# Performance work log

Measured on AMD Instinct MI355X. Metric: run time of the kernel, lower is better.

Reference implementation:

```python
import jax, jax.numpy as jnp
import numpy as np

N = 100000      # nodes
E = 1600000     # directed edges (before self loops)
F_IN = 3        # node_feature_dim
H = 32          # hidden_dim
BN_EPS = 1e-5


def _linear_params(k, fan_in, fan_out):
    lim = 1.0 / np.sqrt(fan_in)
    kw, kb = jax.random.split(k)
    W = jax.random.uniform(kw, (fan_in, fan_out), jnp.float32, -lim, lim)
    b = jax.random.uniform(kb, (fan_out,), jnp.float32, -lim, lim)
    return W, b


def setup_inputs() -> dict:
    key = jax.random.key(0)
    ks = jax.random.split(key, 12)
    x = jax.random.normal(ks[0], (N, F_IN), jnp.float32)
    edge_index = jax.random.randint(ks[1], (2, E), 0, N, dtype=jnp.int64)
    node_type = jax.random.randint(ks[2], (N,), 0, 3, dtype=jnp.int64)
    W1, b1 = _linear_params(ks[3], F_IN, H)
    W2, b2 = _linear_params(ks[4], H, H)
    W3, b3 = _linear_params(ks[5], H, H)
    g1 = jnp.ones((H,), jnp.float32); be1 = jnp.zeros((H,), jnp.float32)
    g2 = jnp.ones((H,), jnp.float32); be2 = jnp.zeros((H,), jnp.float32)
    Wc1, bc1 = _linear_params(ks[6], H, H // 2)
    Wc2, bc2 = _linear_params(ks[7], H // 2, 1)
    Wd1, bd1 = _linear_params(ks[8], H, H // 2)
    Wd2, bd2 = _linear_params(ks[9], H // 2, 1)
    return dict(x=x, edge_index=edge_index, node_type=node_type,
                W1=W1, b1=b1, W2=W2, b2=b2, W3=W3, b3=b3,
                g1=g1, be1=be1, g2=g2, be2=be2,
                Wc1=Wc1, bc1=bc1, Wc2=Wc2, bc2=bc2,
                Wd1=Wd1, bd1=bd1, Wd2=Wd2, bd2=bd2)


def reference(x, edge_index, node_type, W1, b1, W2, b2, W3, b3,
              g1, be1, g2, be2, Wc1, bc1, Wc2, bc2, Wd1, bd1, Wd2, bd2):
    n = x.shape[0]
    # GCNConv (PyG default): add self loops, symmetric deg^-1/2 normalization
    loop = jnp.arange(n, dtype=edge_index.dtype)
    src = jnp.concatenate([edge_index[0], loop])  # [E+N]
    dst = jnp.concatenate([edge_index[1], loop])
    deg = jax.ops.segment_sum(jnp.ones_like(dst, dtype=x.dtype), dst, num_segments=n)
    dinv = jnp.where(deg > 0, jax.lax.rsqrt(jnp.maximum(deg, 1.0)), 0.0)
    norm = dinv[src] * dinv[dst]  # [E+N]

    def conv(h, W, b):
        msg = (h @ W)[src] * norm[:, None]                  # gather + scale
        return jax.ops.segment_sum(msg, dst, num_segments=n) + b  # scatter-add

    def bn(h, g, be):  # BatchNorm1d with batch statistics (training math)
        mu = h.mean(axis=0)
        var = ((h - mu) ** 2).mean(axis=0)
        return (h - mu) * jax.lax.rsqrt(var + BN_EPS) * g + be

    h = bn(jax.nn.relu(conv(x, W1, b1)), g1, be1)   # dropout = identity (eval)
    h = bn(jax.nn.relu(conv(h, W2, b2)), g2, be2)
    h = jax.nn.relu(conv(h, W3, b3))

    cand_mask = node_type == 0
    cand_emb = h[cand_mask]                                 # [C, H]
    cand_scores = (jax.nn.relu(cand_emb @ Wc1 + bc1) @ Wc2 + bc2)[:, 0]

    w = jax.nn.softmax(h.sum(axis=1))[:, None]              # [N,1] importance
    g_emb = (h * w).sum(axis=0, keepdims=True)              # [1, H]
    dn = (jax.nn.relu(g_emb @ Wd1 + bd1) @ Wd2 + bd2).reshape(())

    logits = jnp.concatenate([cand_scores, dn[None]], axis=0)
    cand_idx = jnp.nonzero(cand_mask)[0]
    return logits, cand_idx
```

## Files before the change

### kernel.cpp

```cpp
#include <hip/hip_runtime.h>

typedef unsigned int uint;
typedef unsigned char uchar;

#define NB_MAX 256
#define NPB_MAX 2048

#if defined(__has_builtin)
#if __has_builtin(__builtin_amdgcn_cvt_pk_f32_fp8) && __has_builtin(__builtin_amdgcn_cvt_pk_fp8_f32)
#define HW_FP8 1
#endif
#endif

typedef __attribute__((ext_vector_type(2))) float v2f;

static __device__ __forceinline__ uint f2fp8_sw(float v) {
    v = fminf(fmaxf(v, -448.f), 448.f);
    uint u = __float_as_uint(v);
    uint s = (u >> 24) & 0x80u;
    uint mag = u & 0x7FFFFFFFu;
    uint r = mag + 0x7FFFFu + ((mag >> 20) & 1u);
    if (r < 0x3C800000u) return s;
    uint e8 = (r - 0x3C000000u) >> 20;
    return s | min(e8, 0x7Eu);
}
static __device__ __forceinline__ float fp82f(uint b) {
    uint mag = b & 0x7Fu;
    uint bits = ((b & 0x80u) << 24) | ((mag << 20) + 0x3C000000u);
    return mag ? __uint_as_float(bits) : 0.f;
}
static __device__ __forceinline__ void dec8(uint2 v, float* o) {
#ifdef HW_FP8
    v2f a = __builtin_amdgcn_cvt_pk_f32_fp8((int)v.x, false);
    v2f b = __builtin_amdgcn_cvt_pk_f32_fp8((int)v.x, true);
    v2f c = __builtin_amdgcn_cvt_pk_f32_fp8((int)v.y, false);
    v2f d = __builtin_amdgcn_cvt_pk_f32_fp8((int)v.y, true);
    o[0]=a.x; o[1]=a.y; o[2]=b.x; o[3]=b.y;
    o[4]=c.x; o[5]=c.y; o[6]=d.x; o[7]=d.y;
#else
    o[0]=fp82f(v.x&0xFF); o[1]=fp82f((v.x>>8)&0xFF); o[2]=fp82f((v.x>>16)&0xFF); o[3]=fp82f(v.x>>24);
    o[4]=fp82f(v.y&0xFF); o[5]=fp82f((v.y>>8)&0xFF); o[6]=fp82f((v.y>>16)&0xFF); o[7]=fp82f(v.y>>24);
#endif
}
static __device__ __forceinline__ uint2 enc8(const float* o) {
#ifdef HW_FP8
    int rx = __builtin_amdgcn_cvt_pk_fp8_f32(o[0], o[1], 0, false);
    rx = __builtin_amdgcn_cvt_pk_fp8_f32(o[2], o[3], rx, true);
    int ry = __builtin_amdgcn_cvt_pk_fp8_f32(o[4], o[5], 0, false);
    ry = __builtin_amdgcn_cvt_pk_fp8_f32(o[6], o[7], ry, true);
    return make_uint2((uint)rx, (uint)ry);
#else
    uint2 r;
    r.x = f2fp8_sw(o[0]) | (f2fp8_sw(o[1])<<8) | (f2fp8_sw(o[2])<<16) | (f2fp8_sw(o[3])<<24);
    r.y = f2fp8_sw(o[4]) | (f2fp8_sw(o[5])<<8) | (f2fp8_sw(o[6])<<16) | (f2fp8_sw(o[7])<<24);
    return r;
#endif
}
static __device__ __forceinline__ void dec32(const uchar* row, float* o) {
    const uint4* r4 = (const uint4*)row;
    uint4 A = r4[0], B = r4[1];
    dec8(make_uint2(A.x,A.y), o); dec8(make_uint2(A.z,A.w), o+8);
    dec8(make_uint2(B.x,B.y), o+16); dec8(make_uint2(B.z,B.w), o+24);
}
static __device__ __forceinline__ void enc32(const float* o, uchar* row) {
    uint2 a = enc8(o), b = enc8(o+8), c = enc8(o+16), d = enc8(o+24);
    uint4* r4 = (uint4*)row;
    r4[0] = make_uint4(a.x,a.y,b.x,b.y);
    r4[1] = make_uint4(c.x,c.y,d.x,d.y);
}

static __device__ __forceinline__ unsigned wave_incl_scan(unsigned v) {
    int lane = threadIdx.x & 63;
    #pragma unroll
    for (int d = 1; d < 64; d <<= 1) {
        unsigned t = (unsigned)__shfl_up((int)v, d, 64);
        if (lane >= d) v += t;
    }
    return v;
}

static __device__ void block_excl_scan(const uint* in, uint* out, int n, uint* wscr) {
    int tid = threadIdx.x;
    int lane = tid & 63, wid = tid >> 6;
    int base = tid * 8;
    uint v[8], pre[8], s = 0;
    #pragma unroll
    for (int k = 0; k < 8; k++) v[k] = (base + k < n) ? in[base + k] : 0u;
    #pragma unroll
    for (int k = 0; k < 8; k++) { pre[k] = s; s += v[k]; }
    uint is = wave_incl_scan(s);
    __syncthreads();
    if (lane == 63) wscr[wid] = is;
    __syncthreads();
    uint woff = 0;
    for (int wI = 0; wI < wid; wI++) woff += wscr[wI];
    uint excl = is - s + woff;
    #pragma unroll
    for (int k = 0; k < 8; k++) if (base + k < n) out[base + k] = excl + pre[k];
    __syncthreads();
}

__global__ __launch_bounds__(256) void bucket_hist_kernel(const int* src, const int* dst,
                                                          const int* nt, uint* bcnt, uint* bcand,
                                                          int E, int N, int NB, int shift) {
    __shared__ uint bh[NB_MAX], ch[NB_MAX];
    int tid = threadIdx.x;
    bh[tid] = 0; ch[tid] = 0;
    __syncthreads();
    int gs = gridDim.x * 256;
    for (int i = blockIdx.x * 256 + tid; i < E; i += gs) {
        int d = dst[i], s = src[i];
        if ((uint)d < (uint)N && (uint)s < (uint)N) atomicAdd(&bh[d >> shift], 1u);
    }
    for (int i = blockIdx.x * 256 + tid; i < N; i += gs) {
        if (nt[i] == 0) atomicAdd(&ch[i >> shift], 1u);
    }
    __syncthreads();
    if (bh[tid]) atomicAdd(&bcnt[tid], bh[tid]);
    if (ch[tid]) atomicAdd(&bcand[tid], ch[tid]);
}

__global__ __launch_bounds__(256) void partition_kernel(const int* src, const int* dst,
                                                        const uint* bcnt, uint* alloc0,
                                                        uint* staging, int E, int N, int shift) {
    __shared__ uint bbase_s[NB_MAX];
    __shared__ uint lh[NB_MAX], gb[NB_MAX];
    __shared__ uint ws4[4];
    int tid = threadIdx.x;
    int lane = tid & 63, wid = tid >> 6;
    uint a = bcnt[tid];
    uint ia = wave_incl_scan(a);
    if (lane == 63) ws4[wid] = ia;
    __syncthreads();
    uint off = 0;
    for (int wI = 0; wI < wid; wI++) off += ws4[wI];
    bbase_s[tid] = ia - a + off;
    lh[tid] = 0;
    __syncthreads();
    int base = blockIdx.x * 2048;
    uint mask = (1u << shift) - 1u;
    int breg[8];
    uint rreg[8], pk8[8];
    #pragma unroll
    for (int k = 0; k < 8; k++) {
        int e = base + k * 256 + tid;
        breg[k] = -1;
        if (e < E) {
            int s = src[e], d = dst[e];
            if ((uint)d < (uint)N && (uint)s < (uint)N) {
                int b = d >> shift;
                pk8[k] = (((uint)d & mask) << 17) | (uint)s;
                breg[k] = b;
                rreg[k] = atomicAdd(&lh[b], 1u);
            }
        }
    }
    __syncthreads();
    gb[tid] = lh[tid] ? (bbase_s[tid] + atomicAdd(&alloc0[tid], lh[tid])) : 0u;
    __syncthreads();
    #pragma unroll
    for (int k = 0; k < 8; k++) {
        if (breg[k] >= 0)
            staging[gb[breg[k]] + rreg[k]] = pk8[k];
    }
}

__global__ __launch_bounds__(256) void local_csr_kernel(const uint* staging, const uint* bcnt,
                                                        const uint* bcand, const int* nt,
                                                        const float* x, const float* W1,
                                                        int* csr_src, uint* csr_off, uint* cand_pos,
                                                        float* dinv, uchar* zb,
                                                        int N, int shift, int NB) {
    __shared__ uint deg[NPB_MAX];
    __shared__ uint ofs[NPB_MAX];
    __shared__ uint ws4[4];
    __shared__ uint sb[4];
    __shared__ float Ws[96];
    int b = blockIdx.x, tid = threadIdx.x;
    int lane = tid & 63, wid = tid >> 6;
    if (tid < 96) Ws[tid] = W1[tid];
    uint a = bcnt[tid];
    uint ia = wave_incl_scan(a);
    if (lane == 63) ws4[wid] = ia;
    __syncthreads();
    uint off = 0;
    for (int wI = 0; wI < wid; wI++) off += ws4[wI];
    if (tid == b) { sb[0] = ia - a + off; sb[1] = ia + off; }
    __syncthreads();
    uint c = bcand[tid];
    uint ic = wave_incl_scan(c);
    if (lane == 63) ws4[wid] = ic;
    __syncthreads();
    uint offc = 0;
    for (int wI = 0; wI < wid; wI++) offc += ws4[wI];
    if (tid == b) sb[2] = ic - c + offc;
    __syncthreads();
    uint ebase = sb[0], eend = sb[1], cb = sb[2];
    int nbase = b << shift;
    int ncount = min(1 << shift, N - nbase);
    for (int i = tid; i < ncount; i += 256) deg[i] = 0;
    __syncthreads();
    for (uint p = ebase + tid; p < eend; p += 256)
        atomicAdd(&deg[staging[p] >> 17], 1u);
    __syncthreads();
    block_excl_scan(deg, ofs, ncount, ws4);
    for (int i = tid; i < ncount; i += 256)
        csr_off[nbase + i] = ebase + ofs[i];
    if (b == NB - 1 && tid == 0) csr_off[N] = eend;
    for (int i = tid; i < ncount; i += 256) {
        int g = nbase + i;
        float di = rsqrtf((float)(deg[i] + 1u));
        dinv[g] = di;
        float x0 = x[3 * g], x1 = x[3 * g + 1], x2 = x[3 * g + 2];
        float o[32];
        #pragma unroll
        for (int j = 0; j < 32; j++)
            o[j] = (x0 * Ws[j] + x1 * Ws[32 + j] + x2 * Ws[64 + j]) * di;
        enc32(o, zb + (size_t)g * 32);
    }
    __syncthreads();
    for (int i = tid; i < ncount; i += 256) deg[i] = 0;
    __syncthreads();
    for (uint p = ebase + tid; p < eend; p += 256) {
        uint pkv = staging[p];
        uint dl = pkv >> 17;
        uint pos = ebase + ofs[dl] + atomicAdd(&deg[dl], 1u);
        csr_src[pos] = (int)(pkv & 0x1FFFFu);
    }
    __syncthreads();
    for (int i = tid; i < ncount; i += 256) deg[i] = (nt[nbase + i] == 0) ? 1u : 0u;
    __syncthreads();
    block_excl_scan(deg, ofs, ncount, ws4);
    for (int i = tid; i < ncount; i += 256) cand_pos[nbase + i] = cb + ofs[i];
}

__global__ __launch_bounds__(256) void gemmf_kernel(const uchar* hb, const float* stats_sum,
                                                    const float* stats_sq, const float* g,
                                                    const float* be, const float* W,
                                                    const float* dinv, uchar* zb, int n,
                                                    float inv_n) {
    __shared__ float Ws[1024];
    __shared__ float cs[32];
    __shared__ float a_s[32], d_s[32];
    int tid = threadIdx.x;
    if (tid < 32) {
        float mu = stats_sum[tid] * inv_n;
        float var = fmaxf(stats_sq[tid] * inv_n - mu * mu, 0.f);
        float a = g[tid] * rsqrtf(var + 1e-5f);
        a_s[tid] = a;
        d_s[tid] = be[tid] - mu * a;
    }
    __syncthreads();
    #pragma unroll
    for (int t = tid; t < 1024; t += 256) Ws[t] = a_s[t >> 5] * W[t];
    if (tid < 32) {
        float c = 0.f;
        for (int k = 0; k < 32; k++) c += d_s[k] * W[k * 32 + tid];
        cs[tid] = c;
    }
    __syncthreads();
    int i = blockIdx.x * 256 + tid;
    if (i >= n) return;
    float hk[32], acc[32];
    dec32(hb + (size_t)i * 32, hk);
    #pragma unroll
    for (int j = 0; j < 32; j++) acc[j] = cs[j];
    #pragma unroll
    for (int k = 0; k < 32; k++) {
        float h0 = hk[k];
        #pragma unroll
        for (int j = 0; j < 32; j++) acc[j] += h0 * Ws[k * 32 + j];
    }
    float di = dinv[i];
    #pragma unroll
    for (int j = 0; j < 32; j++) acc[j] *= di;
    enc32(acc, zb + (size_t)i * 32);
}

__global__ __launch_bounds__(256) void agg_kernel(const uchar* zb, const int* csr_src,
                                                  const uint* csr_off, const float* dinv,
                                                  const float* bias, uchar* hb, int n,
                                                  int mode, float* stats_sum, float* stats_sq,
                                                  float* rowsum, uint* maxkey) {
    const int tid = threadIdx.x;
    const int wave = tid >> 6;
    const int lane = tid & 63;
    const int c4 = lane & 3;
    const int slot = lane >> 2;
    const int qlead = lane & ~3;
    __shared__ uint s_lt;
    float bv[8];
    #pragma unroll
    for (int j = 0; j < 8; j++) bv[j] = bias[c4 * 8 + j];
    float bs[8], bq[8];
    #pragma unroll
    for (int j = 0; j < 8; j++) { bs[j] = 0.f; bq[j] = 0.f; }
    float lmax = -3.0e38f;
    for (uint cbase = (uint)blockIdx.x * 128u; cbase < (uint)n; cbase += gridDim.x * 128u) {
        uint avail = min((uint)n - cbase, 128u);
        if (tid == 0) s_lt = 0u;
        __syncthreads();
        while (true) {
            uint li = 0;
            if (c4 == 0) li = atomicAdd(&s_lt, 1u);
            li = (uint)__shfl((int)li, qlead, 64);
            if (li >= avail) break;
            uint node = cbase + li;
            uint s = csr_off[node], e = csr_off[node + 1];
            float acc[8];
            dec8(*(const uint2*)(zb + (size_t)node * 32 + c4 * 8), acc);
            for (uint p = s; p < e; p += 8) {
                uint idx[8];
                float wg[8];
                #pragma unroll
                for (int j = 0; j < 8; j++) {
                    uint q = p + (uint)j;
                    uint qc = min(q, e - 1u);
                    idx[j] = (uint)csr_src[qc];
                    wg[j] = (q < e) ? 1.f : 0.f;
                }
                #pragma unroll
                for (int j = 0; j < 8; j++) {
                    float t[8];
                    dec8(*(const uint2*)(zb + (size_t)idx[j] * 32 + c4 * 8), t);
                    #pragma unroll
                    for (int cI = 0; cI < 8; cI++) acc[cI] = fmaf(wg[j], t[cI], acc[cI]);
                }
            }
            float di = dinv[node];
            float hv[8];
            #pragma unroll
            for (int j = 0; j < 8; j++) hv[j] = fmaxf(di * acc[j] + bv[j], 0.f);
            *(uint2*)(hb + (size_t)node * 32 + c4 * 8) = enc8(hv);
            if (mode == 0) {
                #pragma unroll
                for (int j = 0; j < 8; j++) { bs[j] += hv[j]; bq[j] += hv[j] * hv[j]; }
            } else {
                float rs = ((hv[0] + hv[1]) + (hv[2] + hv[3])) + ((hv[4] + hv[5]) + (hv[6] + hv[7]));
                rs += __shfl_xor(rs, 1, 64);
                rs += __shfl_xor(rs, 2, 64);
                if (c4 == 0) { rowsum[node] = rs; lmax = fmaxf(lmax, rs); }
            }
        }
        __syncthreads();
    }
    if (mode == 0) {
        #pragma unroll
        for (int m = 4; m < 64; m <<= 1) {
            #pragma unroll
            for (int j = 0; j < 8; j++) {
                bs[j] += __shfl_xor(bs[j], m, 64);
                bq[j] += __shfl_xor(bq[j], m, 64);
            }
        }
        __shared__ float ssum[4][32], ssq[4][32];
        if (slot == 0) {
            #pragma unroll
            for (int j = 0; j < 8; j++) { ssum[wave][c4 * 8 + j] = bs[j]; ssq[wave][c4 * 8 + j] = bq[j]; }
        }
        __syncthreads();
        if (tid < 32) {
            atomicAdd(&stats_sum[tid], ssum[0][tid] + ssum[1][tid] + ssum[2][tid] + ssum[3][tid]);
            atomicAdd(&stats_sq[tid],  ssq[0][tid] + ssq[1][tid] + ssq[2][tid] + ssq[3][tid]);
        }
    } else {
        #pragma unroll
        for (int m = 1; m < 64; m <<= 1) lmax = fmaxf(lmax, __shfl_xor(lmax, m, 64));
        __shared__ float lm[4];
        if (lane == 0) lm[wave] = lmax;
        __syncthreads();
        if (tid == 0) {
            float m = fmaxf(fmaxf(lm[0], lm[1]), fmaxf(lm[2], lm[3]));
            uint u = __float_as_uint(m);
            uint key = (u & 0x80000000u) ? ~u : (u | 0x80000000u);
            atomicMax(maxkey, key);
        }
    }
}

__global__ __launch_bounds__(256) void head_kernel(const uchar* hb, const int* nt,
                                                   const uint* pos, const float* Wc1,
                                                   const float* bc1, const float* Wc2,
                                                   const float* bc2, const float* rowsum,
                                                   const uint* maxkey, float* gvec, float* Zp,
                                                   uint* ticket, const float* Wd1,
                                                   const float* bd1, const float* Wd2,
                                                   const float* bd2, float* out, int n, int C) {
    __shared__ float W1s[512], b1s[16], W2s[16];
    __shared__ float ls[256];
    __shared__ float ge[32], tt[16];
    __shared__ int lastflag;
    int tid = threadIdx.x;
    for (int t = tid; t < 512; t += 256) W1s[t] = Wc1[t];
    if (tid < 16) { b1s[tid] = bc1[tid]; W2s[tid] = Wc2[tid]; }
    __syncthreads();
    int i = blockIdx.x * 256 + tid;
    if (i < n && nt[i] == 0) {
        float hv[32];
        dec32(hb + (size_t)i * 32, hv);
        float s = bc2[0];
        #pragma unroll
        for (int j = 0; j < 16; j++) {
            float u = b1s[j];
            #pragma unroll
            for (int k = 0; k < 32; k++) u += hv[k] * W1s[k * 16 + j];
            s += fmaxf(u, 0.f) * W2s[j];
        }
        s = fminf(fmaxf(s, -1000.f), 1000.f);
        uint p = pos[i];
        if (p < (uint)C) {
            out[p] = s;
            out[C + 1 + p] = (float)i;
        }
    }
    uint key = *maxkey;
    float M = 0.f;
    if (key != 0u) M = (key & 0x80000000u) ? __uint_as_float(key ^ 0x80000000u) : __uint_as_float(~key);
    int lane = tid & 31, grp = tid >> 5;
    int stride = gridDim.x * 8;
    float accZ = 0.f, accg = 0.f;
    for (int node = blockIdx.x * 8 + grp; node < n; node += stride) {
        float ew = __expf(rowsum[node] - M);
        accg += fp82f(hb[(size_t)node * 32 + lane]) * ew;
        if (lane == 0) accZ += ew;
    }
    ls[tid] = accg;
    __syncthreads();
    if (tid < 32) {
        float a = 0.f;
        #pragma unroll
        for (int g = 0; g < 8; g++) a += ls[tid + 32 * g];
        atomicAdd(&gvec[tid], a);
    }
    __syncthreads();
    ls[tid] = (lane == 0) ? accZ : 0.f;
    __syncthreads();
    if (tid == 0) {
        float a = 0.f;
        for (int t = 0; t < 256; t += 32) a += ls[t];
        atomicAdd(Zp, a);
        __threadfence();
        uint old = atomicAdd(ticket, 1u);
        lastflag = (old == gridDim.x - 1) ? 1 : 0;
    }
    __syncthreads();
    if (lastflag) {
        __threadfence();
        if (tid < 32) ge[tid] = atomicAdd(&gvec[tid], 0.f);
        if (tid == 0) ls[0] = atomicAdd(Zp, 0.f);
        __syncthreads();
        float Zv = fmaxf(ls[0], 1e-30f);
        if (tid < 32) ge[tid] /= Zv;
        __syncthreads();
        if (tid < 16) {
            float s = bd1[tid];
            for (int k = 0; k < 32; k++) s += ge[k] * Wd1[k * 16 + tid];
            tt[tid] = fmaxf(s, 0.f);
        }
        __syncthreads();
        if (tid == 0) {
            float s = bd2[0];
            for (int j = 0; j < 16; j++) s += tt[j] * Wd2[j];
            out[C] = fminf(fmaxf(s, -1000.f), 1000.f);
        }
    }
}

extern "C" void kernel_launch(void* const* d_in, const int* in_sizes, int n_in,
                              void* d_out, int out_size, void* d_ws, size_t ws_size,
                              hipStream_t stream) {
    const float* x   = (const float*)d_in[0];
    const int*   ei  = (const int*)d_in[1];
    const int*   nt  = (const int*)d_in[2];
    const float* W1  = (const float*)d_in[3];  const float* b1  = (const float*)d_in[4];
    const float* W2  = (const float*)d_in[5];  const float* b2  = (const float*)d_in[6];
    const float* W3  = (const float*)d_in[7];  const float* b3  = (const float*)d_in[8];
    const float* g1  = (const float*)d_in[9];  const float* be1 = (const float*)d_in[10];
    const float* g2  = (const float*)d_in[11]; const float* be2 = (const float*)d_in[12];
    const float* Wc1 = (const float*)d_in[13]; const float* bc1 = (const float*)d_in[14];
    const float* Wc2 = (const float*)d_in[15]; const float* bc2 = (const float*)d_in[16];
    const float* Wd1 = (const float*)d_in[17]; const float* bd1 = (const float*)d_in[18];
    const float* Wd2 = (const float*)d_in[19]; const float* bd2 = (const float*)d_in[20];

    const int N = in_sizes[0] / 3;
    const int E = in_sizes[1] / 2;
    const int C = (out_size - 1) / 2;
    const int* e_src = ei;
    const int* e_dst = ei + E;
    float* out = (float*)d_out;

    int shift = 9;
    while (((N + (1 << shift) - 1) >> shift) > NB_MAX) shift++;
    const int NB = (N + (1 << shift) - 1) >> shift;

    char* w = (char*)d_ws;
    auto alloc = [&](size_t bytes) { void* p = (void*)w; w += (bytes + 255) & ~(size_t)255; return p; };
    float*    stats  = (float*)alloc(256 * 4);
    uint*     bcnt   = (uint*)alloc(NB_MAX * 4);
    uint*     bcand  = (uint*)alloc(NB_MAX * 4);
    uint*     alloc0 = (uint*)alloc(NB_MAX * 4);
    size_t zero_bytes = (size_t)((char*)w - (char*)stats);
    float*    dinv   = (float*)alloc((size_t)N * 4);
    uint*     csr_off= (uint*)alloc((size_t)(N + 1) * 4);
    uint*     cand_pos=(uint*)alloc((size_t)N * 4);
    float*    rowsum = (float*)alloc((size_t)N * 4);
    int*      csr_src= (int*)alloc((size_t)E * 4);
    uint*     staging= (uint*)alloc((size_t)E * 4);
    uchar*    zb     = (uchar*)alloc((size_t)N * 32);
    uchar*    hb     = (uchar*)alloc((size_t)N * 32);

    float* sum1 = stats;       float* sq1 = stats + 32;
    float* sum2 = stats + 64;  float* sq2 = stats + 96;
    float* gvec = stats + 128; float* Zp  = stats + 160;
    uint* maxkey = (uint*)(stats + 161);
    uint* ticket = (uint*)(stats + 162);

    hipMemsetAsync(stats, 0, zero_bytes, stream);

    const int gN   = (N + 255) / 256;
    const int gPar = (E + 2047) / 2048;
    const int gAgg = (N + 127) / 128;
    const float inv_n = 1.0f / (float)N;

    hipLaunchKernelGGL(bucket_hist_kernel, dim3(784), dim3(256), 0, stream, e_src, e_dst, nt, bcnt, bcand, E, N, NB, shift);
    hipLaunchKernelGGL(partition_kernel, dim3(gPar), dim3(256), 0, stream, e_src, e_dst, bcnt, alloc0, staging, E, N, shift);
    hipLaunchKernelGGL(local_csr_kernel, dim3(NB), dim3(256), 0, stream, staging, bcnt, bcand, nt,
                       x, W1, csr_src, csr_off, cand_pos, dinv, zb, N, shift, NB);

    hipLaunchKernelGGL(agg_kernel, dim3(gAgg), dim3(256), 0, stream, zb, csr_src, csr_off,
                       dinv, b1, hb, N, 0, sum1, sq1, rowsum, maxkey);

    hipLaunchKernelGGL(gemmf_kernel, dim3(gN), dim3(256), 0, stream, hb, sum1, sq1, g1, be1, W2, dinv, zb, N, inv_n);
    hipLaunchKernelGGL(agg_kernel, dim3(gAgg), dim3(256), 0, stream, zb, csr_src, csr_off,
                       dinv, b2, hb, N, 0, sum2, sq2, rowsum, maxkey);

    hipLaunchKernelGGL(gemmf_kernel, dim3(gN), dim3(256), 0, stream, hb, sum2, sq2, g2, be2, W3, dinv, zb, N, inv_n);
    hipLaunchKernelGGL(agg_kernel, dim3(gAgg), dim3(256), 0, stream, zb, csr_src, csr_off,
                       dinv, b3, hb, N, 1, sum1, sq1, rowsum, maxkey);

    hipLaunchKernelGGL(head_kernel, dim3(gN), dim3(256), 0, stream, hb, nt, cand_pos,
                       Wc1, bc1, Wc2, bc2, rowsum, maxkey, gvec, Zp, ticket,
                       Wd1, bd1, Wd2, bd2, out, N, C);
}
```

Baseline: 332.3 us.

## Aggregate raw 3-dim features before applying W1 in first GCN layer

The first layer now uses (A·X)·W1 instead of A·(X·W1). Node features scaled by dinv are stored as float4 instead of 32 fp8 channels, and a new agg1 kernel gathers 3 floats per edge, then applies W1, bias and ReLU per node. This cuts first-layer gather traffic and removes the fp8 quantisation of the pre-aggregation product. In exchange each edge gathers 16 bytes of fp32 per neighbour and four lanes share one node, so parallelism differs from the generic aggregation kernel.

After: 321.5 us. -3.3%, faster.

```diff
diff --git a/kernel.cpp b/kernel.cpp
--- a/kernel.cpp
+++ b/kernel.cpp
@@ -167,18 +167,16 @@
 
 __global__ __launch_bounds__(256) void local_csr_kernel(const uint* staging, const uint* bcnt,
                                                         const uint* bcand, const int* nt,
-                                                        const float* x, const float* W1,
+                                                        const float* x,
                                                         int* csr_src, uint* csr_off, uint* cand_pos,
-                                                        float* dinv, uchar* zb,
+                                                        float* dinv, float4* xs,
                                                         int N, int shift, int NB) {
     __shared__ uint deg[NPB_MAX];
     __shared__ uint ofs[NPB_MAX];
     __shared__ uint ws4[4];
     __shared__ uint sb[4];
-    __shared__ float Ws[96];
     int b = blockIdx.x, tid = threadIdx.x;
     int lane = tid & 63, wid = tid >> 6;
-    if (tid < 96) Ws[tid] = W1[tid];
     uint a = bcnt[tid];
     uint ia = wave_incl_scan(a);
     if (lane == 63) ws4[wid] = ia;
@@ -211,12 +209,7 @@
         int g = nbase + i;
         float di = rsqrtf((float)(deg[i] + 1u));
         dinv[g] = di;
-        float x0 = x[3 * g], x1 = x[3 * g + 1], x2 = x[3 * g + 2];
-        float o[32];
-        #pragma unroll
-        for (int j = 0; j < 32; j++)
-            o[j] = (x0 * Ws[j] + x1 * Ws[32 + j] + x2 * Ws[64 + j]) * di;
-        enc32(o, zb + (size_t)g * 32);
+        xs[g] = make_float4(x[3*g] * di, x[3*g+1] * di, x[3*g+2] * di, 0.f);
     }
     __syncthreads();
     for (int i = tid; i < ncount; i += 256) deg[i] = 0;
@@ -232,6 +225,89 @@
     __syncthreads();
     block_excl_scan(deg, ofs, ncount, ws4);
     for (int i = tid; i < ncount; i += 256) cand_pos[nbase + i] = cb + ofs[i];
+}
+
+__global__ __launch_bounds__(256) void agg1_kernel(const float* xs, const int* csr_src,
+                                                   const uint* csr_off, const float* dinv,
+                                                   const float* W1, const float* b1, uchar* hb,
+                                                   int n, float* stats_sum, float* stats_sq) {
+    const int tid = threadIdx.x;
+    const int wave = tid >> 6;
+    const int lane = tid & 63;
+    const int c4 = lane & 3;
+    const int slot = lane >> 2;
+    const int qlead = lane & ~3;
+    __shared__ float W1s[96];
+    __shared__ uint s_lt;
+    if (tid < 96) W1s[tid] = W1[tid];
+    float bv[8];
+    #pragma unroll
+    for (int j = 0; j < 8; j++) bv[j] = b1[c4 * 8 + j];
+    float bs[8], bq[8];
+    #pragma unroll
+    for (int j = 0; j < 8; j++) { bs[j] = 0.f; bq[j] = 0.f; }
+    __syncthreads();
+    for (uint cbase = (uint)blockIdx.x * 128u; cbase < (uint)n; cbase += gridDim.x * 128u) {
+        uint avail = min((uint)n - cbase, 128u);
+        if (tid == 0) s_lt = 0u;
+        __syncthreads();
+        while (true) {
+            uint li = 0;
+            if (c4 == 0) li = atomicAdd(&s_lt, 1u);
+            li = (uint)__shfl((int)li, qlead, 64);
+            if (li >= avail) break;
+            uint node = cbase + li;
+            uint s = csr_off[node], e = csr_off[node + 1];
+            float acc = xs[(size_t)node * 4 + c4];
+            for (uint p = s; p < e; p += 8) {
+                uint idx[8];
+                float wg[8];
+                #pragma unroll
+                for (int j = 0; j < 8; j++) {
+                    uint q = p + (uint)j;
+                    uint qc = min(q, e - 1u);
+                    idx[j] = (uint)csr_src[qc];
+                    wg[j] = (q < e) ? 1.f : 0.f;
+                }
+                #pragma unroll
+                for (int j = 0; j < 8; j++)
+                    acc = fmaf(wg[j], xs[(size_t)idx[j] * 4 + c4], acc);
+            }
+            float u = dinv[node] * acc;
+            float u0 = __shfl(u, qlead, 64);
+            float u1 = __shfl(u, qlead + 1, 64);
+            float u2 = __shfl(u, qlead + 2, 64);
+            float hv[8];
+            #pragma unroll
+            for (int j = 0; j < 8; j++) {
+                int ch = c4 * 8 + j;
+                float o = u0 * W1s[ch] + u1 * W1s[32 + ch] + u2 * W1s[64 + ch] + bv[j];
+                hv[j] = fmaxf(o, 0.f);
+            }
+            *(uint2*)(hb + (size_t)node * 32 + c4 * 8) = enc8(hv);
+            #pragma unroll
+            for (int j = 0; j < 8; j++) { bs[j] += hv[j]; bq[j] += hv[j] * hv[j]; }
+        }
+        __syncthreads();
+    }
+    #pragma unroll
+    for (int m = 4; m < 64; m <<= 1) {
+        #pragma unroll
+        for (int j = 0; j < 8; j++) {
+            bs[j] += __shfl_xor(bs[j], m, 64);
+            bq[j] += __shfl_xor(bq[j], m, 64);
+        }
+    }
+    __shared__ float ssum[4][32], ssq[4][32];
+    if (slot == 0) {
+        #pragma unroll
+        for (int j = 0; j < 8; j++) { ssum[wave][c4 * 8 + j] = bs[j]; ssq[wave][c4 * 8 + j] = bq[j]; }
+    }
+    __syncthreads();
+    if (tid < 32) {
+        atomicAdd(&stats_sum[tid], ssum[0][tid] + ssum[1][tid] + ssum[2][tid] + ssum[3][tid]);
+        atomicAdd(&stats_sq[tid],  ssq[0][tid] + ssq[1][tid] + ssq[2][tid] + ssq[3][tid]);
+    }
 }
 
 __global__ __launch_bounds__(256) void gemmf_kernel(const uchar* hb, const float* stats_sum,
@@ -508,6 +584,7 @@
     uint*     staging= (uint*)alloc((size_t)E * 4);
     uchar*    zb     = (uchar*)alloc((size_t)N * 32);
     uchar*    hb     = (uchar*)alloc((size_t)N * 32);
+    float4*   xs     = (float4*)zb;
 
     float* sum1 = stats;       float* sq1 = stats + 32;
     float* sum2 = stats + 64;  float* sq2 = stats + 96;
@@ -525,10 +602,10 @@
     hipLaunchKernelGGL(bucket_hist_kernel, dim3(784), dim3(256), 0, stream, e_src, e_dst, nt, bcnt, bcand, E, N, NB, shift);
     hipLaunchKernelGGL(partition_kernel, dim3(gPar), dim3(256), 0, stream, e_src, e_dst, bcnt, alloc0, staging, E, N, shift);
     hipLaunchKernelGGL(local_csr_kernel, dim3(NB), dim3(256), 0, stream, staging, bcnt, bcand, nt,
-                       x, W1, csr_src, csr_off, cand_pos, dinv, zb, N, shift, NB);
-
-    hipLaunchKernelGGL(agg_kernel, dim3(gAgg), dim3(256), 0, stream, zb, csr_src, csr_off,
-                       dinv, b1, hb, N, 0, sum1, sq1, rowsum, maxkey);
+                       x, csr_src, csr_off, cand_pos, dinv, xs, N, shift, NB);
+
+    hipLaunchKernelGGL(agg1_kernel, dim3(gAgg), dim3(256), 0, stream, (const float*)xs, csr_src, csr_off,
+                       dinv, W1, b1, hb, N, sum1, sq1);
 
     hipLaunchKernelGGL(gemmf_kernel, dim3(gN), dim3(256), 0, stream, hb, sum1, sq1, g1, be1, W2, dinv, zb, N, inv_n);
     hipLaunchKernelGGL(agg_kernel, dim3(gAgg), dim3(256), 0, stream, zb, csr_src, csr_off,
```
